# Optimization experiments

Measured on AMD Instinct MI355X. Metric: run time of the kernel, lower is better.

The kernel has to match this reference:

```python
import jax, jax.numpy as jnp
import numpy as np

EPS = 1e-12  # torch F.normalize eps

def _normalize(v):
    return v / jnp.maximum(jnp.linalg.norm(v, axis=-1, keepdims=True), EPS)

def setup_inputs() -> dict:
    key = jax.random.key(0)
    ks = jax.random.split(key, 8)
    N, K, D = 500000, 32, 3
    positions = jax.random.normal(ks[0], (N, D), dtype=jnp.float32)
    neighbors = jax.random.normal(ks[1], (N, K, D), dtype=jnp.float32)
    # tiny MLP params: Linear(D,5) -> ReLU -> Linear(5,5) -> ReLU -> Linear(5,1)
    s1 = 1.0 / np.sqrt(D)
    s2 = 1.0 / np.sqrt(5)
    W1 = jax.random.uniform(ks[2], (5, D), jnp.float32, -s1, s1)
    b1 = jax.random.uniform(ks[3], (5,), jnp.float32, -s1, s1)
    W2 = jax.random.uniform(ks[4], (5, 5), jnp.float32, -s2, s2)
    b2 = jax.random.uniform(ks[5], (5,), jnp.float32, -s2, s2)
    W3 = jax.random.uniform(ks[6], (1, 5), jnp.float32, -s2, s2)
    b3 = jax.random.uniform(ks[7], (1,), jnp.float32, -s2, s2)
    return {"positions": positions, "neighbors": neighbors,
            "W1": W1, "b1": b1, "W2": W2, "b2": b2, "W3": W3, "b3": b3}

def reference(positions, neighbors, W1, b1, W2, b2, W3, b3):
    # [N,K,D] normalized neighbor difference vectors
    diffs = neighbors - positions[:, None, :]
    nd = _normalize(diffs)
    # tiny MLP producing a scalar weight per neighbor
    h = jax.nn.relu(jnp.einsum('nkd,hd->nkh', nd, W1) + b1)
    h = jax.nn.relu(jnp.einsum('nkh,gh->nkg', h, W2) + b2)
    w = jnp.einsum('nkh,oh->nko', h, W3) + b3  # [N,K,1]
    vel = jnp.sum(nd * w, axis=1)  # [N,D]
    return _normalize(vel)
```

## Files before the change

### kernel.cpp

```cpp
#include <hip/hip_runtime.h>


#define K 32

__global__ __launch_bounds__(256) void velvec_kernel(
    const float* __restrict__ pos,
    const float* __restrict__ nbr,
    const float* __restrict__ W1,
    const float* __restrict__ b1,
    const float* __restrict__ W2,
    const float* __restrict__ b2,
    const float* __restrict__ W3,
    const float* __restrict__ b3,
    float* __restrict__ out,
    int N)
{
    const int point = blockIdx.x * blockDim.x + threadIdx.x;
    if (point >= N) return;

    float w1[5][3], bb1[5], w2[5][5], bb2[5], w3[5];
#pragma unroll
    for (int h = 0; h < 5; ++h) {
        bb1[h] = b1[h];
        bb2[h] = b2[h];
        w3[h]  = W3[h];
#pragma unroll
        for (int d = 0; d < 3; ++d) w1[h][d] = W1[h * 3 + d];
#pragma unroll
        for (int g = 0; g < 5; ++g) w2[h][g] = W2[h * 5 + g];
    }
    const float bb3 = b3[0];

    const float px = pos[point * 3 + 0];
    const float py = pos[point * 3 + 1];
    const float pz = pos[point * 3 + 2];

    const float4* nb4 = (const float4*)(nbr + (size_t)point * (K * 3));

    float vx = 0.0f, vy = 0.0f, vz = 0.0f;

#pragma unroll
    for (int c = 0; c < 8; ++c) {
        const float4 f0 = nb4[c * 3 + 0];
        const float4 f1 = nb4[c * 3 + 1];
        const float4 f2 = nb4[c * 3 + 2];
        float nx[4], ny[4], nz[4];
        nx[0] = f0.x; ny[0] = f0.y; nz[0] = f0.z;
        nx[1] = f0.w; ny[1] = f1.x; nz[1] = f1.y;
        nx[2] = f1.z; ny[2] = f1.w; nz[2] = f2.x;
        nx[3] = f2.y; ny[3] = f2.z; nz[3] = f2.w;

#pragma unroll
        for (int j = 0; j < 4; ++j) {
            float dx = nx[j] - px;
            float dy = ny[j] - py;
            float dz = nz[j] - pz;
            float n2 = dx * dx + dy * dy + dz * dz;
            float inv = (n2 > 1e-24f) ? __builtin_amdgcn_rsqf(n2) : 1e12f;
            dx *= inv; dy *= inv; dz *= inv;

            float h1[5];
#pragma unroll
            for (int h = 0; h < 5; ++h) {
                float a = bb1[h];
                a = fmaf(w1[h][0], dx, a);
                a = fmaf(w1[h][1], dy, a);
                a = fmaf(w1[h][2], dz, a);
                h1[h] = fmaxf(a, 0.0f);
            }
            float h2[5];
#pragma unroll
            for (int g = 0; g < 5; ++g) {
                float a = bb2[g];
#pragma unroll
                for (int h = 0; h < 5; ++h) a = fmaf(w2[g][h], h1[h], a);
                h2[g] = fmaxf(a, 0.0f);
            }
            float w = bb3;
#pragma unroll
            for (int h = 0; h < 5; ++h) w = fmaf(w3[h], h2[h], w);

            vx = fmaf(dx, w, vx);
            vy = fmaf(dy, w, vy);
            vz = fmaf(dz, w, vz);
        }
    }

    float vn2  = vx * vx + vy * vy + vz * vz;
    float vinv = (vn2 > 1e-24f) ? __builtin_amdgcn_rsqf(vn2) : 1e12f;
    out[point * 3 + 0] = vx * vinv;
    out[point * 3 + 1] = vy * vinv;
    out[point * 3 + 2] = vz * vinv;
}

extern "C" void kernel_launch(void* const* d_in, const int* in_sizes, int n_in,
                              void* d_out, int out_size, void* d_ws, size_t ws_size,
                              hipStream_t stream) {
    const float* pos = (const float*)d_in[0];
    const float* nbr = (const float*)d_in[1];
    const float* W1  = (const float*)d_in[2];
    const float* b1  = (const float*)d_in[3];
    const float* W2  = (const float*)d_in[4];
    const float* b2  = (const float*)d_in[5];
    const float* W3  = (const float*)d_in[6];
    const float* b3  = (const float*)d_in[7];
    float* out = (float*)d_out;

    const int N = in_sizes[0] / 3;
    const int threads = 256;
    const int blocks = (N + threads - 1) / threads;

    velvec_kernel<<<blocks, threads, 0, stream>>>(pos, nbr, W1, b1, W2, b2, W3, b3,
                                                  out, N);
}
```

Baseline: 294.5 us.

## Stage neighbor data through LDS with coalesced loads and split points across four lanes

```diff
diff --git a/kernel.cpp b/kernel.cpp
--- a/kernel.cpp
+++ b/kernel.cpp
@@ -2,6 +2,9 @@
 
 
 #define K 32
+#define PTS_PER_BLOCK 64
+#define F4_PER_PT 24
+#define F4_STRIDE 25
 
 __global__ __launch_bounds__(256) void velvec_kernel(
     const float* __restrict__ pos,
@@ -15,8 +18,25 @@
     float* __restrict__ out,
     int N)
 {
-    const int point = blockIdx.x * blockDim.x + threadIdx.x;
-    if (point >= N) return;
+    __shared__ float4 lds4[PTS_PER_BLOCK * F4_STRIDE];
+
+    const int t = threadIdx.x;
+
+    const int   pt_base     = blockIdx.x * PTS_PER_BLOCK;
+    const int   pts_in_blk  = min(PTS_PER_BLOCK, N - pt_base);
+    const int   valid4      = pts_in_blk * F4_PER_PT;
+    const long long base4   = (long long)pt_base * F4_PER_PT;
+    const float4* __restrict__ nbr4 = (const float4*)nbr;
+
+#pragma unroll
+    for (int i = 0; i < 6; ++i) {
+        int idx = t + i * 256;
+        if (idx < valid4) {
+            unsigned pp = (unsigned)idx / F4_PER_PT;
+            unsigned e  = (unsigned)idx % F4_PER_PT;
+            lds4[pp * F4_STRIDE + e] = nbr4[base4 + idx];
+        }
+    }
 
     float w1[5][3], bb1[5], w2[5][5], bb2[5], w3[5];
 #pragma unroll
@@ -31,66 +51,73 @@
     }
     const float bb3 = b3[0];
 
-    const float px = pos[point * 3 + 0];
-    const float py = pos[point * 3 + 1];
-    const float pz = pos[point * 3 + 2];
+    __syncthreads();
 
-    const float4* nb4 = (const float4*)(nbr + (size_t)point * (K * 3));
+    const int p_local = t >> 2;
+    const int sub     = t & 3;
+    const int p       = pt_base + p_local;
+    if (p >= N) return;
+
+    const float px = pos[p * 3 + 0];
+    const float py = pos[p * 3 + 1];
+    const float pz = pos[p * 3 + 2];
+
+    float4 f[6];
+#pragma unroll
+    for (int j = 0; j < 6; ++j)
+        f[j] = lds4[p_local * F4_STRIDE + sub * 6 + j];
+    const float* a = (const float*)f;
 
     float vx = 0.0f, vy = 0.0f, vz = 0.0f;
 
 #pragma unroll
-    for (int c = 0; c < 8; ++c) {
-        const float4 f0 = nb4[c * 3 + 0];
-        const float4 f1 = nb4[c * 3 + 1];
-        const float4 f2 = nb4[c * 3 + 2];
-        float nx[4], ny[4], nz[4];
-        nx[0] = f0.x; ny[0] = f0.y; nz[0] = f0.z;
-        nx[1] = f0.w; ny[1] = f1.x; nz[1] = f1.y;
-        nx[2] = f1.z; ny[2] = f1.w; nz[2] = f2.x;
-        nx[3] = f2.y; ny[3] = f2.z; nz[3] = f2.w;
+    for (int j = 0; j < 8; ++j) {
+        float dx = a[j * 3 + 0] - px;
+        float dy = a[j * 3 + 1] - py;
+        float dz = a[j * 3 + 2] - pz;
+        float n2 = dx * dx + dy * dy + dz * dz;
+        float inv = (n2 > 1e-24f) ? __builtin_amdgcn_rsqf(n2) : 1e12f;
+        dx *= inv; dy *= inv; dz *= inv;
+
+        float h1[5];
+#pragma unroll
+        for (int h = 0; h < 5; ++h) {
+            float acc = bb1[h];
+            acc = fmaf(w1[h][0], dx, acc);
+            acc = fmaf(w1[h][1], dy, acc);
+            acc = fmaf(w1[h][2], dz, acc);
+            h1[h] = fmaxf(acc, 0.0f);
+        }
+        float h2[5];
+#pragma unroll
+        for (int g = 0; g < 5; ++g) {
+            float acc = bb2[g];
+#pragma unroll
+            for (int h = 0; h < 5; ++h) acc = fmaf(w2[g][h], h1[h], acc);
+            h2[g] = fmaxf(acc, 0.0f);
+        }
+        float w = bb3;
+#pragma unroll
+        for (int h = 0; h < 5; ++h) w = fmaf(w3[h], h2[h], w);
+
+        vx = fmaf(dx, w, vx);
+        vy = fmaf(dy, w, vy);
+        vz = fmaf(dz, w, vz);
+    }
 
 #pragma unroll
-        for (int j = 0; j < 4; ++j) {
-            float dx = nx[j] - px;
-            float dy = ny[j] - py;
-            float dz = nz[j] - pz;
-            float n2 = dx * dx + dy * dy + dz * dz;
-            float inv = (n2 > 1e-24f) ? __builtin_amdgcn_rsqf(n2) : 1e12f;
-            dx *= inv; dy *= inv; dz *= inv;
-
-            float h1[5];
-#pragma unroll
-            for (int h = 0; h < 5; ++h) {
-                float a = bb1[h];
-                a = fmaf(w1[h][0], dx, a);
-                a = fmaf(w1[h][1], dy, a);
-                a = fmaf(w1[h][2], dz, a);
-                h1[h] = fmaxf(a, 0.0f);
-            }
-            float h2[5];
-#pragma unroll
-            for (int g = 0; g < 5; ++g) {
-                float a = bb2[g];
-#pragma unroll
-                for (int h = 0; h < 5; ++h) a = fmaf(w2[g][h], h1[h], a);
-                h2[g] = fmaxf(a, 0.0f);
-            }
-            float w = bb3;
-#pragma unroll
-            for (int h = 0; h < 5; ++h) w = fmaf(w3[h], h2[h], w);
-
-            vx = fmaf(dx, w, vx);
-            vy = fmaf(dy, w, vy);
-            vz = fmaf(dz, w, vz);
-        }
+    for (int m = 1; m <= 2; m <<= 1) {
+        vx += __shfl_xor(vx, m, 4);
+        vy += __shfl_xor(vy, m, 4);
+        vz += __shfl_xor(vz, m, 4);
     }
 
     float vn2  = vx * vx + vy * vy + vz * vz;
     float vinv = (vn2 > 1e-24f) ? __builtin_amdgcn_rsqf(vn2) : 1e12f;
-    out[point * 3 + 0] = vx * vinv;
-    out[point * 3 + 1] = vy * vinv;
-    out[point * 3 + 2] = vz * vinv;
+    if (sub < 3) {
+        float c = (sub == 0) ? vx : (sub == 1) ? vy : vz;
+        out[p * 3 + sub] = c * vinv;
+    }
 }
 
 extern "C" void kernel_launch(void* const* d_in, const int* in_sizes, int n_in,
@@ -107,9 +134,8 @@
     float* out = (float*)d_out;
 
     const int N = in_sizes[0] / 3;
-    const int threads = 256;
-    const int blocks = (N + threads - 1) / threads;
+    const int blocks = (N + PTS_PER_BLOCK - 1) / PTS_PER_BLOCK;
 
-    velvec_kernel<<<blocks, threads, 0, stream>>>(pos, nbr, W1, b1, W2, b2, W3, b3,
-                                                  out, N);
+    velvec_kernel<<<blocks, 256, 0, stream>>>(pos, nbr, W1, b1, W2, b2, W3, b3,
+                                              out, N);
 }
```

After: 289.0 us. No clear change (-1.8%).
